# Kernel tuning notes

Hardware: AMD Instinct MI355X
Metric: run time of the kernel (lower is better)

The kernel has to match this reference:

```python
import jax, jax.numpy as jnp
import numpy as np

RADIUS = 1.0
NSAMPLE = 32


def _query_ball(new_xyz, xyz, radius, nsample):
    # new_xyz (B,M,3), xyz (B,N,3) -> idx (B,M,nsample) int32
    B, M, _ = new_xyz.shape
    N = xyz.shape[1]
    # squared distances via ||q||^2 + ||p||^2 - 2 q.p (avoids BxMxNx3 diff tensor)
    q2 = jnp.sum(new_xyz * new_xyz, axis=-1)          # (B,M)
    p2 = jnp.sum(xyz * xyz, axis=-1)                  # (B,N)
    qp = jnp.einsum('bmd,bnd->bmn', new_xyz, xyz)     # (B,M,N)
    dist2 = q2[:, :, None] + p2[:, None, :] - 2.0 * qp
    mask = dist2 < radius * radius
    ar = jnp.arange(N, dtype=jnp.int32)
    masked = jnp.where(mask, ar[None, None, :], jnp.int32(N + 1))  # (B,M,N)
    first = jnp.sort(masked, axis=2)[:, :, :nsample]               # (B,M,S)
    first_valid = first[:, :, :1]                                   # pad with first neighbor
    idx = jnp.where(first == N + 1, first_valid, first)
    return idx.astype(jnp.int32)


def _group(points, idx):
    # points (B,C,N), idx (B,M,S) -> (B,C,M,S) gather along N
    B, C, N = points.shape
    M, S = idx.shape[1], idx.shape[2]
    ie = jnp.broadcast_to(idx.reshape(B, 1, M * S).astype(jnp.int32), (B, C, M * S))
    return jnp.take_along_axis(points, ie, axis=2).reshape(B, C, M, S)


def setup_inputs() -> dict:
    key = jax.random.key(0)
    k1, k2 = jax.random.split(key)
    B, N, M, C = 8, 8192, 2048, 64
    xyz = jax.random.normal(k1, (B, N, 3), dtype=jnp.float32)
    # centroids are a subset of the cloud -> every ball query has >= 1 valid neighbor
    new_xyz = xyz[:, :M, :]
    features = jax.random.normal(k2, (B, C, N), dtype=jnp.float32)
    return {"xyz": xyz, "new_xyz": new_xyz, "features": features}


def reference(xyz, new_xyz, features):
    idx = _query_ball(new_xyz, xyz, RADIUS, NSAMPLE)                      # (B,M,S)
    grouped_xyz = _group(jnp.swapaxes(xyz, 1, 2), idx)                    # (B,3,M,S)
    grouped_xyz = grouped_xyz - jnp.swapaxes(new_xyz, 1, 2)[..., None]    # recenter
    grouped_feat = _group(features, idx)                                  # (B,C,M,S)
    return jnp.concatenate([grouped_xyz, grouped_feat], axis=1)           # (B,3+C,M,S)
```

## Files before the change

kernel.cpp:

```cpp
#include <hip/hip_runtime.h>

#define N_PTS 8192
#define M_Q   2048
#define C_F   64
#define NS    32
#define B_SZ  8

__global__ __launch_bounds__(256) void prep_kernel(
    const float* __restrict__ feat, const float* __restrict__ xyz,
    float* __restrict__ featT, float4* __restrict__ xyz4)
{
#pragma clang fp contract(off)
    __shared__ float lds[C_F * 65];
    if (blockIdx.x < B_SZ * 128) {
        const int b  = blockIdx.x >> 7;
        const int n0 = (blockIdx.x & 127) * 64;
        {
            const int c4 = threadIdx.x >> 6;
            const int nn = threadIdx.x & 63;
#pragma unroll
            for (int k = 0; k < 16; ++k) {
                const int c = k * 4 + c4;
                lds[c * 65 + nn] = feat[((size_t)b * C_F + c) * N_PTS + n0 + nn];
            }
        }
        __syncthreads();
        {
            const int n4 = threadIdx.x >> 6;
            const int c  = threadIdx.x & 63;
#pragma unroll
            for (int k = 0; k < 16; ++k) {
                const int nn = k * 4 + n4;
                featT[((size_t)b * N_PTS + n0 + nn) * C_F + c] = lds[c * 65 + nn];
            }
        }
    } else {
        const int i = (blockIdx.x - B_SZ * 128) * 256 + (int)threadIdx.x;
        const float p0 = xyz[i * 3 + 0];
        const float p1 = xyz[i * 3 + 1];
        const float p2 = xyz[i * 3 + 2];
        const float s  = (p0 * p0 + p1 * p1) + p2 * p2;
        xyz4[i] = make_float4(p0, p1, p2, s);
    }
}

__global__ __launch_bounds__(256) void qbg_kernel(
    const float4* __restrict__ xyz4, const float* __restrict__ nxyz,
    const float* __restrict__ featT, float* __restrict__ out)
{
#pragma clang fp contract(off)
    __shared__ int   sidx[4][NS];
    __shared__ float stage[67 * 33];

    const int lane = threadIdx.x & 63;
    const int w    = threadIdx.x >> 6;
    const int q    = blockIdx.x * 4 + w;
    const int b    = q >> 11;
    const float4* __restrict__ xb = xyz4 + (size_t)b * N_PTS;

    {
        const float* __restrict__ qp = nxyz + (size_t)q * 3;
        const float qx = qp[0], qy = qp[1], qz = qp[2];
        const float q2 = (qx * qx + qy * qy) + qz * qz;

        int  cnt = 0;
        int  first_idx = 0;
        bool have_first = false;

        for (int base = 0; base < N_PTS && cnt < NS; base += 256) {
            float4 P[4];
#pragma unroll
            for (int cc = 0; cc < 4; ++cc)
                P[cc] = xb[base + cc * 64 + lane];
#pragma unroll
            for (int cc = 0; cc < 4; ++cc) {
                if (cnt >= NS) break;
                const float qpdot = (qx * P[cc].x + qy * P[cc].y) + qz * P[cc].z;
                const float d2 = (q2 + P[cc].w) - 2.0f * qpdot;
                const bool pred = d2 < 1.0f;
                const unsigned long long mask = __ballot(pred);
                if (mask) {
                    if (!have_first) {
                        first_idx = base + cc * 64 + __ffsll(mask) - 1;
                        have_first = true;
                    }
                    if (pred) {
                        const int pos = cnt + (int)__popcll(mask & ((1ull << lane) - 1ull));
                        if (pos < NS) sidx[w][pos] = base + cc * 64 + lane;
                    }
                    cnt += (int)__popcll(mask);
                }
            }
        }
        if (cnt < NS) {
            for (int p = cnt + lane; p < NS; p += 64) sidx[w][p] = first_idx;
        }
    }
    __syncthreads();

    const int pS = threadIdx.x >> 3;
    const int j  = threadIdx.x & 7;
    const size_t cstride = (size_t)M_Q * NS;

    for (int w2 = 0; w2 < 4; ++w2) {
        const int qq = blockIdx.x * 4 + w2;
        const int mm = qq & (M_Q - 1);
        const int n  = sidx[w2][pS];

        const float* __restrict__ fb = featT + ((size_t)b * N_PTS + n) * C_F;
#pragma unroll
        for (int k = 0; k < 2; ++k) {
            const int c = k * 32 + j * 4;
            const float4 v = *(const float4*)(fb + c);
            stage[(3 + c + 0) * 33 + pS] = v.x;
            stage[(3 + c + 1) * 33 + pS] = v.y;
            stage[(3 + c + 2) * 33 + pS] = v.z;
            stage[(3 + c + 3) * 33 + pS] = v.w;
        }
        if (j == 0) {
            const float4 pv = xb[n];
            const float* __restrict__ qp2 = nxyz + (size_t)qq * 3;
            stage[0 * 33 + pS] = pv.x - qp2[0];
            stage[1 * 33 + pS] = pv.y - qp2[1];
            stage[2 * 33 + pS] = pv.z - qp2[2];
        }
        __syncthreads();

        const size_t obase = ((size_t)b * 67 * M_Q + mm) * NS;
#pragma unroll
        for (int it = 0; it < 3; ++it) {
            const int e = it * 256 + (int)threadIdx.x;
            if (e < 67 * 8) {
                const int row  = e >> 3;
                const int col4 = (e & 7) * 4;
                float4 v;
                v.x = stage[row * 33 + col4 + 0];
                v.y = stage[row * 33 + col4 + 1];
                v.z = stage[row * 33 + col4 + 2];
                v.w = stage[row * 33 + col4 + 3];
                *(float4*)&out[obase + (size_t)row * cstride + col4] = v;
            }
        }
        __syncthreads();
    }
}

extern "C" void kernel_launch(void* const* d_in, const int* in_sizes, int n_in,
                              void* d_out, int out_size, void* d_ws, size_t ws_size,
                              hipStream_t stream)
{
    const float* xyz  = (const float*)d_in[0];
    const float* nxyz = (const float*)d_in[1];
    const float* feat = (const float*)d_in[2];
    float* out = (float*)d_out;

    float*  featT = (float*)d_ws;
    float4* xyz4  = (float4*)((char*)d_ws + (20 << 20));

    const int Q = B_SZ * M_Q;

    prep_kernel<<<B_SZ * 128 + (B_SZ * N_PTS) / 256, 256, 0, stream>>>(
        feat, xyz, featT, xyz4);
    qbg_kernel<<<Q / 4, 256, 0, stream>>>(xyz4, nxyz, featT, out);
}
```

Before: 178.2 us.

## Split ball query and gather; gather per channel plane from LDS

Splits the fused query-and-group kernel into a scan kernel that writes neighbor indices to global memory and a gather kernel. The gather kernel loads one whole channel plane of 8192 floats into LDS and serves random reads from it. This drops the feature transpose pass and the scattered global gathers of feature rows. In exchange, each index tile is re-read once per channel, every block loads a 32 KB plane, and there is an extra launch plus an index round-trip through global memory.

Measured after the change: 208.8 us. 1.17x slower.

```diff
diff --git a/kernel.cpp b/kernel.cpp
--- a/kernel.cpp
+++ b/kernel.cpp
@@ -6,142 +6,156 @@
 #define NS    32
 #define B_SZ  8
 
+
 __global__ __launch_bounds__(256) void prep_kernel(
-    const float* __restrict__ feat, const float* __restrict__ xyz,
-    float* __restrict__ featT, float4* __restrict__ xyz4)
+    const float* __restrict__ xyz, const float* __restrict__ nxyz,
+    float4* __restrict__ xyz4, float* __restrict__ xyzT,
+    float* __restrict__ nxyzT)
 {
 #pragma clang fp contract(off)
-    __shared__ float lds[C_F * 65];
-    if (blockIdx.x < B_SZ * 128) {
-        const int b  = blockIdx.x >> 7;
-        const int n0 = (blockIdx.x & 127) * 64;
-        {
-            const int c4 = threadIdx.x >> 6;
-            const int nn = threadIdx.x & 63;
-#pragma unroll
-            for (int k = 0; k < 16; ++k) {
-                const int c = k * 4 + c4;
-                lds[c * 65 + nn] = feat[((size_t)b * C_F + c) * N_PTS + n0 + nn];
-            }
-        }
-        __syncthreads();
-        {
-            const int n4 = threadIdx.x >> 6;
-            const int c  = threadIdx.x & 63;
-#pragma unroll
-            for (int k = 0; k < 16; ++k) {
-                const int nn = k * 4 + n4;
-                featT[((size_t)b * N_PTS + n0 + nn) * C_F + c] = lds[c * 65 + nn];
-            }
-        }
-    } else {
-        const int i = (blockIdx.x - B_SZ * 128) * 256 + (int)threadIdx.x;
+    const int i = blockIdx.x * 256 + (int)threadIdx.x;
+    if (i < B_SZ * N_PTS) {
         const float p0 = xyz[i * 3 + 0];
         const float p1 = xyz[i * 3 + 1];
         const float p2 = xyz[i * 3 + 2];
         const float s  = (p0 * p0 + p1 * p1) + p2 * p2;
         xyz4[i] = make_float4(p0, p1, p2, s);
+        const int b = i >> 13;
+        const int n = i & (N_PTS - 1);
+        xyzT[((size_t)b * 3 + 0) * N_PTS + n] = p0;
+        xyzT[((size_t)b * 3 + 1) * N_PTS + n] = p1;
+        xyzT[((size_t)b * 3 + 2) * N_PTS + n] = p2;
+    } else {
+        const int j = i - B_SZ * N_PTS;
+        const float q0 = nxyz[j * 3 + 0];
+        const float q1 = nxyz[j * 3 + 1];
+        const float q2 = nxyz[j * 3 + 2];
+        const int b = j >> 11;
+        const int m = j & (M_Q - 1);
+        nxyzT[((size_t)b * 3 + 0) * M_Q + m] = q0;
+        nxyzT[((size_t)b * 3 + 1) * M_Q + m] = q1;
+        nxyzT[((size_t)b * 3 + 2) * M_Q + m] = q2;
     }
 }
 
-__global__ __launch_bounds__(256) void qbg_kernel(
+__global__ __launch_bounds__(256) void scan_kernel(
     const float4* __restrict__ xyz4, const float* __restrict__ nxyz,
-    const float* __restrict__ featT, float* __restrict__ out)
+    int* __restrict__ gidx)
 {
 #pragma clang fp contract(off)
-    __shared__ int   sidx[4][NS];
-    __shared__ float stage[67 * 33];
-
     const int lane = threadIdx.x & 63;
     const int w    = threadIdx.x >> 6;
     const int q    = blockIdx.x * 4 + w;
     const int b    = q >> 11;
     const float4* __restrict__ xb = xyz4 + (size_t)b * N_PTS;
+    int* __restrict__ gout = gidx + (size_t)q * NS;
+
+    const float* __restrict__ qp = nxyz + (size_t)q * 3;
+    const float qx = qp[0], qy = qp[1], qz = qp[2];
+    const float q2 = (qx * qx + qy * qy) + qz * qz;
+
+    int  cnt = 0;
+    int  first_idx = 0;
+    bool have_first = false;
+
+    for (int base = 0; base < N_PTS && cnt < NS; base += 256) {
+        float4 P[4];
+#pragma unroll
+        for (int cc = 0; cc < 4; ++cc)
+            P[cc] = xb[base + cc * 64 + lane];
+#pragma unroll
+        for (int cc = 0; cc < 4; ++cc) {
+            if (cnt >= NS) break;
+            const float qpdot = (qx * P[cc].x + qy * P[cc].y) + qz * P[cc].z;
+            const float d2 = (q2 + P[cc].w) - 2.0f * qpdot;
+            const bool pred = d2 < 1.0f;
+            const unsigned long long mask = __ballot(pred);
+            if (mask) {
+                if (!have_first) {
+                    first_idx = base + cc * 64 + __ffsll(mask) - 1;
+                    have_first = true;
+                }
+                if (pred) {
+                    const int pos = cnt + (int)__popcll(mask & ((1ull << lane) - 1ull));
+                    if (pos < NS) gout[pos] = base + cc * 64 + lane;
+                }
+                cnt += (int)__popcll(mask);
+            }
+        }
+    }
+    if (cnt < NS) {
+        for (int p = cnt + lane; p < NS; p += 64) gout[p] = first_idx;
+    }
+}
+
+__global__ __launch_bounds__(256) void gather_kernel(
+    const float* __restrict__ feat, const float* __restrict__ xyzT,
+    const float* __restrict__ nxyzT, const int* __restrict__ gidx,
+    float* __restrict__ out)
+{
+#pragma clang fp contract(off)
+    __shared__ float plane[N_PTS];
+    __shared__ float qsh[512];
+
+    const int x   = blockIdx.x & 7;
+    const int t   = blockIdx.x >> 3;
+    const int gq  = t / 67;
+    const int c   = t % 67;
+    const int gid = gq * 8 + x;
+    const int b   = gid >> 2;
+    const int mq  = gid & 3;
+    const int m0  = mq * 512;
+
+    const float* __restrict__ src =
+        (c < 3) ? (xyzT + ((size_t)b * 3 + c) * N_PTS)
+                : (feat + ((size_t)b * C_F + (c - 3)) * N_PTS);
 
     {
-        const float* __restrict__ qp = nxyz + (size_t)q * 3;
-        const float qx = qp[0], qy = qp[1], qz = qp[2];
-        const float q2 = (qx * qx + qy * qy) + qz * qz;
-
-        int  cnt = 0;
-        int  first_idx = 0;
-        bool have_first = false;
-
-        for (int base = 0; base < N_PTS && cnt < NS; base += 256) {
-            float4 P[4];
+        const float4* __restrict__ s4 = (const float4*)src;
+        float4* p4 = (float4*)plane;
 #pragma unroll
-            for (int cc = 0; cc < 4; ++cc)
-                P[cc] = xb[base + cc * 64 + lane];
-#pragma unroll
-            for (int cc = 0; cc < 4; ++cc) {
-                if (cnt >= NS) break;
-                const float qpdot = (qx * P[cc].x + qy * P[cc].y) + qz * P[cc].z;
-                const float d2 = (q2 + P[cc].w) - 2.0f * qpdot;
-                const bool pred = d2 < 1.0f;
-                const unsigned long long mask = __ballot(pred);
-                if (mask) {
-                    if (!have_first) {
-                        first_idx = base + cc * 64 + __ffsll(mask) - 1;
-                        have_first = true;
-                    }
-                    if (pred) {
-                        const int pos = cnt + (int)__popcll(mask & ((1ull << lane) - 1ull));
-                        if (pos < NS) sidx[w][pos] = base + cc * 64 + lane;
-                    }
-                    cnt += (int)__popcll(mask);
-                }
-            }
-        }
-        if (cnt < NS) {
-            for (int p = cnt + lane; p < NS; p += 64) sidx[w][p] = first_idx;
-        }
+        for (int k = 0; k < 8; ++k)
+            p4[k * 256 + threadIdx.x] = s4[k * 256 + threadIdx.x];
+    }
+    if (c < 3) {
+        const float* __restrict__ qsrc = nxyzT + ((size_t)b * 3 + c) * M_Q + m0;
+        qsh[threadIdx.x]       = qsrc[threadIdx.x];
+        qsh[256 + threadIdx.x] = qsrc[256 + threadIdx.x];
     }
     __syncthreads();
 
-    const int pS = threadIdx.x >> 3;
-    const int j  = threadIdx.x & 7;
-    const size_t cstride = (size_t)M_Q * NS;
+    const int* __restrict__ idxp = gidx + ((size_t)b * M_Q + m0) * NS;
+    float* __restrict__ op = out + (((size_t)b * 67 + c) * M_Q + m0) * NS;
 
-    for (int w2 = 0; w2 < 4; ++w2) {
-        const int qq = blockIdx.x * 4 + w2;
-        const int mm = qq & (M_Q - 1);
-        const int n  = sidx[w2][pS];
-
-        const float* __restrict__ fb = featT + ((size_t)b * N_PTS + n) * C_F;
-#pragma unroll
-        for (int k = 0; k < 2; ++k) {
-            const int c = k * 32 + j * 4;
-            const float4 v = *(const float4*)(fb + c);
-            stage[(3 + c + 0) * 33 + pS] = v.x;
-            stage[(3 + c + 1) * 33 + pS] = v.y;
-            stage[(3 + c + 2) * 33 + pS] = v.z;
-            stage[(3 + c + 3) * 33 + pS] = v.w;
+    if (c < 3) {
+#pragma unroll 4
+        for (int it = 0; it < 16; ++it) {
+            const int e  = it * 256 + (int)threadIdx.x;
+            const int m  = e >> 3;
+            const int s4 = (e & 7) * 4;
+            const int4 nn = *(const int4*)(idxp + m * NS + s4);
+            const float qc = qsh[m];
+            float4 v;
+            v.x = plane[nn.x] - qc;
+            v.y = plane[nn.y] - qc;
+            v.z = plane[nn.z] - qc;
+            v.w = plane[nn.w] - qc;
+            *(float4*)(op + (size_t)m * NS + s4) = v;
         }
-        if (j == 0) {
-            const float4 pv = xb[n];
-            const float* __restrict__ qp2 = nxyz + (size_t)qq * 3;
-            stage[0 * 33 + pS] = pv.x - qp2[0];
-            stage[1 * 33 + pS] = pv.y - qp2[1];
-            stage[2 * 33 + pS] = pv.z - qp2[2];
+    } else {
+#pragma unroll 4
+        for (int it = 0; it < 16; ++it) {
+            const int e  = it * 256 + (int)threadIdx.x;
+            const int m  = e >> 3;
+            const int s4 = (e & 7) * 4;
+            const int4 nn = *(const int4*)(idxp + m * NS + s4);
+            float4 v;
+            v.x = plane[nn.x];
+            v.y = plane[nn.y];
+            v.z = plane[nn.z];
+            v.w = plane[nn.w];
+            *(float4*)(op + (size_t)m * NS + s4) = v;
         }
-        __syncthreads();
-
-        const size_t obase = ((size_t)b * 67 * M_Q + mm) * NS;
-#pragma unroll
-        for (int it = 0; it < 3; ++it) {
-            const int e = it * 256 + (int)threadIdx.x;
-            if (e < 67 * 8) {
-                const int row  = e >> 3;
-                const int col4 = (e & 7) * 4;
-                float4 v;
-                v.x = stage[row * 33 + col4 + 0];
-                v.y = stage[row * 33 + col4 + 1];
-                v.z = stage[row * 33 + col4 + 2];
-                v.w = stage[row * 33 + col4 + 3];
-                *(float4*)&out[obase + (size_t)row * cstride + col4] = v;
-            }
-        }
-        __syncthreads();
     }
 }
 
@@ -154,12 +168,13 @@
     const float* feat = (const float*)d_in[2];
     float* out = (float*)d_out;
 
-    float*  featT = (float*)d_ws;
-    float4* xyz4  = (float4*)((char*)d_ws + (20 << 20));
+    float4* xyz4  = (float4*)d_ws;
+    float*  xyzT  = (float*)((char*)d_ws + (2u << 20));
+    float*  nxyzT = (float*)((char*)d_ws + (4u << 20));
+    int*    gidx  = (int*)  ((char*)d_ws + (6u << 20));
 
-    const int Q = B_SZ * M_Q;
-
-    prep_kernel<<<B_SZ * 128 + (B_SZ * N_PTS) / 256, 256, 0, stream>>>(
-        feat, xyz, featT, xyz4);
-    qbg_kernel<<<Q / 4, 256, 0, stream>>>(xyz4, nxyz, featT, out);
+    prep_kernel<<<(B_SZ * N_PTS + B_SZ * M_Q) / 256, 256, 0, stream>>>(
+        xyz, nxyz, xyz4, xyzT, nxyzT);
+    scan_kernel<<<(B_SZ * M_Q) / 4, 256, 0, stream>>>(xyz4, nxyz, gidx);
+    gather_kernel<<<B_SZ * 67 * 4, 256, 0, stream>>>(feat, xyzT, nxyzT, gidx, out);
 }
```
